# Kernel optimization log

Hardware: AMD Instinct MI355X
Metric: run time of the kernel (lower is better)

The kernel has to match this reference:

```python
import jax, jax.numpy as jnp
import numpy as np

N = 10000      # atoms
F = 32         # nr_atom_basis
H = 7          # nr_heads
C = F * H      # nr_coefficients = 224
E = 200000     # edges
NRBF = 50
CUTOFF = 5.0
EPS = 1e-8


def _seg_sum(x, idx, n):
    return jax.ops.segment_sum(x, idx, num_segments=n)


def _seg_mean(x, idx, n):
    # torch scatter_reduce 'mean' with include_self=False: sum/count, 0 for empty segments
    s = _seg_sum(x, idx, n)
    cnt = _seg_sum(jnp.ones((x.shape[0],), x.dtype), idx, n)
    cnt = jnp.maximum(cnt, 1.0).reshape((n,) + (1,) * (x.ndim - 1))
    return s / cnt


def _scatter_softmax(w, idx, n):
    m = jax.ops.segment_max(w, idx, num_segments=n)
    m = jnp.where(jnp.isfinite(m), m, 0.0)  # guard empty segments
    e = jnp.exp(w - m[idx])
    s = _seg_sum(e, idx, n)
    return e / s[idx]


def setup_inputs():
    key = jax.random.key(0)
    ks = jax.random.split(key, 16)
    def w(k, shape, scale=0.1):
        return jax.random.normal(k, shape, jnp.float32) * scale
    return {
        "h": w(ks[0], (N, F), 1.0),
        "x": w(ks[1], (N, 3), 1.0),
        "v": w(ks[2], (N, 3), 0.1),
        "pairlist": jax.random.randint(ks[3], (2, E), 0, N),
        "w_in": w(ks[4], (2 * F, NRBF)), "b_in": jnp.zeros((NRBF,), jnp.float32),
        "w_e1": w(ks[5], (2 * F + NRBF + 1, F)), "b_e1": jnp.zeros((F,), jnp.float32),
        "w_e2": w(ks[6], (F, F)), "b_e2": jnp.zeros((F,), jnp.float32),
        "w_att": w(ks[7], (F, H)), "b_att": jnp.zeros((H,), jnp.float32),
        "w_n1": w(ks[8], (F + C + F, F)), "b_n1": jnp.zeros((F,), jnp.float32),
        "w_n2": w(ks[9], (F, F)), "b_n2": jnp.zeros((F,), jnp.float32),
        "w_pn1": w(ks[10], (C, F)), "b_pn1": jnp.zeros((F,), jnp.float32),
        "w_pn2": w(ks[11], (F, F)), "b_pn2": jnp.zeros((F,), jnp.float32),
        "w_v1": w(ks[12], (F, F)), "b_v1": jnp.zeros((F,), jnp.float32),
        "w_v2": w(ks[13], (F, 1)),
        "w_xmix": w(ks[14], (C, C)),
        "w_vmix": w(ks[15], (C, 1)),
    }


def reference(h, x, v, pairlist, w_in, b_in, w_e1, b_e1, w_e2, b_e2,
              w_att, b_att, w_n1, b_n1, w_n2, b_n2, w_pn1, b_pn1,
              w_pn2, b_pn2, w_v1, b_v1, w_v2, w_xmix, w_vmix):
    act = jax.nn.silu
    idx_i, idx_j = pairlist[0], pairlist[1]
    n = h.shape[0]

    r_ij = x[idx_j] - x[idx_i]                      # [E,3]
    d_ij = jnp.linalg.norm(r_ij, axis=-1)           # [E]
    dir_ij = r_ij / (d_ij[:, None] + EPS)           # [E,3]

    # edge model: continuous-filter conv with concatenation
    h_cat = jnp.concatenate([h[idx_i], h[idx_j]], axis=-1)           # [E,2F]
    centers = jnp.linspace(0.0, CUTOFF, NRBF)
    width = centers[1] - centers[0]
    rbf = jnp.exp(-0.5 * ((d_ij[:, None] - centers) / width) ** 2)   # [E,NRBF]
    filt = rbf * (h_cat @ w_in + b_in)                               # [E,NRBF]
    edge_in = jnp.concatenate([h_cat, filt, d_ij[:, None]], axis=-1)
    h_ij_edge = act(edge_in @ w_e1 + b_e1) @ w_e2 + b_e2             # [E,F]

    # semantic attention (scatter softmax over edges grouped by idx_i)
    att_w = jax.nn.celu(h_ij_edge @ w_att + b_att, alpha=2.0)        # [E,H]
    cut = 0.5 * (jnp.cos(jnp.pi * d_ij / CUTOFF) + 1.0) * (d_ij < CUTOFF)
    att = _scatter_softmax(att_w * cut[:, None], idx_i, n)           # [E,H]
    # einsum('pf,ph->pfh').reshape -> f-major, h-minor
    h_ij_sem = (h_ij_edge[:, :, None] * att[:, None, :]).reshape(-1, C)  # [E,C]
    h_i_sem = _seg_sum(h_ij_sem, idx_i, n)                           # [N,C]

    # equivariant combinations + spatial attention
    comb = jnp.tanh(h_ij_sem @ w_xmix)[:, :, None] * dir_ij[:, None, :]  # [E,C,3]
    comb_mean = _seg_mean(comb, idx_i, n)                            # [N,C,3]
    cnsq = jnp.sum(comb_mean ** 2, axis=-1)                          # [N,C]
    h_i_spatial = act(act(cnsq @ w_pn1 + b_pn1) @ w_pn2 + b_pn2)     # [N,F]

    # node update
    node_in = jnp.concatenate([h, h_i_sem, h_i_spatial], axis=-1)
    h_upd = h + act(act(node_in @ w_n1 + b_n1) @ w_n2 + b_n2)        # [N,F]

    # velocity update
    v_ij = jnp.einsum('ecx,c->ex', comb, w_vmix[:, 0])               # [E,3]
    dv = _seg_mean(v_ij, idx_i, n)                                   # [N,3]
    gate = 2.0 * jax.nn.sigmoid(act(h @ w_v1 + b_v1) @ w_v2)         # [N,1]
    v_upd = gate * v + dv
    x_upd = x + v_upd
    return h_upd, x_upd, v_upd
```

## Files before the change

### kernel.cpp

```cpp
#include <hip/hip_runtime.h>
#include <hip/hip_bf16.h>
#include <math.h>

typedef unsigned short u16;
typedef __attribute__((ext_vector_type(8))) short bf16x8;
typedef __attribute__((ext_vector_type(4))) float f32x4;

constexpr int kF    = 32;
constexpr int kH    = 7;
constexpr int kC    = 224;
constexpr int kRBF  = 50;
constexpr int kM    = 128;
constexpr int kStr  = 232;
constexpr int kEM   = 128;
constexpr int kAStr = 136;
constexpr int kBStr = 40;
constexpr float kCut = 5.0f;
constexpr float kEps = 1e-8f;

__device__ __forceinline__ float silu_f(float a) { return a / (1.f + __expf(-a)); }
__device__ __forceinline__ float tanh_f(float x) {
    float e = __expf(2.f * x);
    return 1.f - 2.f / (e + 1.f);
}
__device__ __forceinline__ float bf2f(u16 u) {
    union { unsigned int i; float f; } v; v.i = ((unsigned int)u) << 16; return v.f;
}
__device__ __forceinline__ u16 f2bf(float f) {
    union { float f; unsigned int i; } v; v.f = f;
    unsigned int x = v.i;
    unsigned int round = ((x >> 16) & 1u) + 0x7fffu;
    return (u16)((x + round) >> 16);
}
__device__ __forceinline__ unsigned pk2(float a, float b) {
    union { __hip_bfloat162 h; unsigned u; } v;
    v.h = __float22bfloat162_rn(make_float2(a, b));
    return v.u;
}

__global__ __launch_bounds__(256) void init_kernel(
    const float* __restrict__ wx, const float* __restrict__ w_in,
    const float* __restrict__ w_e1, const float* __restrict__ w_e2,
    const float* __restrict__ w_att, const float* __restrict__ b_e2,
    const float* __restrict__ b_att,
    u16* __restrict__ wxT, u16* __restrict__ W1T, u16* __restrict__ W2T,
    u16* __restrict__ W3T, u16* __restrict__ W24T, float* __restrict__ b24,
    int* __restrict__ counts, int* __restrict__ cursor, int N_)
{
    int idx = blockIdx.x * 256 + threadIdx.x;
    if (idx < kC * kC) {
        int c = idx / kC, k = idx - c * kC;
        wxT[idx] = f2bf(wx[k * kC + c]);
    }
    if (idx < N_) { counts[idx] = 0; cursor[idx] = 0; }

    if (blockIdx.x == 0) {
        int t = threadIdx.x;
        for (int i = t; i < 64 * 64; i += 256) {
            int n = i >> 6, k = i & 63;
            W1T[i] = f2bf((n < kRBF) ? w_in[k * kRBF + n] : 0.f);
        }
        for (int i = t; i < 32 * 128; i += 256) {
            int n = i >> 7, k = i & 127;
            W2T[i] = f2bf((k < 115) ? w_e1[k * kF + n] : 0.f);
        }
        for (int i = t; i < 32 * 32; i += 256) {
            int n = i >> 5, k = i & 31;
            W3T[i] = f2bf(w_e2[k * kF + n]);
        }
        for (int i = t; i < 16 * 32; i += 256) {
            int n = i >> 5, k = i & 31;
            float a = 0.f;
            if (n < kH) for (int o = 0; o < kF; o++) a += w_e2[k * kF + o] * w_att[o * kH + n];
            W24T[i] = f2bf(a);
        }
        if (t < kH) {
            float a = b_att[t];
            for (int o = 0; o < kF; o++) a += b_e2[o] * w_att[o * kH + t];
            b24[t] = a;
        }
    }
}

__global__ __launch_bounds__(256) void hist_kernel(
    const int* __restrict__ pl, int* __restrict__ counts, int E_)
{
    int e = blockIdx.x * 256 + threadIdx.x;
    if (e < E_) atomicAdd(&counts[pl[e]], 1);
}

__global__ __launch_bounds__(1024) void scan_kernel(
    const int* __restrict__ counts, int* __restrict__ offsets, int n)
{
    __shared__ int buf[1024];
    int t = threadIdx.x;
    int chunk = (n + 1023) >> 10;
    int lo = t * chunk;
    int s = 0;
    for (int i = 0; i < chunk; i++) {
        int g = lo + i;
        if (g < n) s += counts[g];
    }
    buf[t] = s;
    __syncthreads();
    for (int off = 1; off < 1024; off <<= 1) {
        int v = (t >= off) ? buf[t - off] : 0;
        __syncthreads();
        buf[t] += v;
        __syncthreads();
    }
    int run = buf[t] - s;
    for (int i = 0; i < chunk; i++) {
        int g = lo + i;
        if (g < n) { offsets[g] = run; run += counts[g]; }
    }
    if (t == 1023) offsets[n] = buf[1023];
}

__global__ __launch_bounds__(256) void scatter_kernel(
    const int* __restrict__ pl, const int* __restrict__ offsets,
    int* __restrict__ cursor, int* __restrict__ rank, int* __restrict__ nid, int E_)
{
    int e = blockIdx.x * 256 + threadIdx.x;
    if (e < E_) {
        int i = pl[e];
        int p = atomicAdd(&cursor[i], 1);
        int pos = offsets[i] + p;
        rank[e] = pos;
        nid[pos] = i;
    }
}

__global__ __launch_bounds__(256) void edge_kernel(
    const float* __restrict__ h, const float* __restrict__ x,
    const int* __restrict__ pl, const int* __restrict__ rank_g, int E_,
    const float* __restrict__ b_in, const float* __restrict__ b_e1,
    const float* __restrict__ b_e2,
    const u16* __restrict__ W1T, const u16* __restrict__ W2T,
    const u16* __restrict__ W3T, const u16* __restrict__ W24T,
    const float* __restrict__ b24,
    float* __restrict__ he_g, float* __restrict__ logit_g,
    float* __restrict__ dir_g)
{
    __shared__ __align__(16) u16 s_A[kEM][kAStr];
    __shared__ __align__(16) u16 s_t1[kEM][kBStr];
    __shared__ float s_d[kEM];
    __shared__ int   s_r[kEM];

    int t = threadIdx.x;
    int T0 = blockIdx.x * kEM;
    int w = t >> 6, lane = t & 63, quad = lane >> 4, l15 = lane & 15;

    {
        int e = t >> 1, half = t & 1;
        int ge = T0 + e;
        bool val = ge < E_;
        int i = 0, j = 0;
        if (val) { i = pl[ge]; j = pl[E_ + ge]; }
        const float4* pi = (const float4*)(h + (size_t)i * kF) + half * 4;
        const float4* pj = (const float4*)(h + (size_t)j * kF) + half * 4;
#pragma unroll
        for (int q = 0; q < 4; q++) {
            float4 a = val ? pi[q] : make_float4(0.f, 0.f, 0.f, 0.f);
            float4 b = val ? pj[q] : make_float4(0.f, 0.f, 0.f, 0.f);
            unsigned* di = (unsigned*)&s_A[e][half * 16 + 4 * q];
            di[0] = pk2(a.x, a.y); di[1] = pk2(a.z, a.w);
            unsigned* dj = (unsigned*)&s_A[e][kF + half * 16 + 4 * q];
            dj[0] = pk2(b.x, b.y); dj[1] = pk2(b.z, b.w);
        }
        if (half == 0) {
            float d = 0.f;
            int r = 0;
            if (val) {
                r = rank_g[ge];
                float r0 = x[j * 3 + 0] - x[i * 3 + 0];
                float r1 = x[j * 3 + 1] - x[i * 3 + 1];
                float r2 = x[j * 3 + 2] - x[i * 3 + 2];
                d = sqrtf(r0 * r0 + r1 * r1 + r2 * r2);
                float inv = 1.0f / (d + kEps);
                dir_g[(size_t)r * 3 + 0] = r0 * inv;
                dir_g[(size_t)r * 3 + 1] = r1 * inv;
                dir_g[(size_t)r * 3 + 2] = r2 * inv;
            }
            s_r[e] = r;
            s_d[e] = d;
            s_A[e][114] = f2bf(d);
            s_A[e][115] = 0;
            unsigned* z = (unsigned*)&s_A[e][116];
#pragma unroll
            for (int q = 0; q < 6; q++) z[q] = 0u;
        }
    }
    __syncthreads();

    const float invw = 49.0f / kCut;

    {
        bf16x8 a1[2][2];
#pragma unroll
        for (int rt = 0; rt < 2; rt++)
#pragma unroll
            for (int kt = 0; kt < 2; kt++)
                a1[rt][kt] = *(const bf16x8*)&s_A[32 * w + 16 * rt + l15][kt * 32 + quad * 8];
#pragma unroll
        for (int ct = 0; ct < 4; ct++) {
            int c = ct * 16 + l15;
            bf16x8 b0 = *(const bf16x8*)(W1T + (size_t)c * 64 + quad * 8);
            bf16x8 b1 = *(const bf16x8*)(W1T + (size_t)c * 64 + 32 + quad * 8);
            float bin = (c < kRBF) ? b_in[c] : 0.f;
#pragma unroll
            for (int rt = 0; rt < 2; rt++) {
                f32x4 acc = {0.f, 0.f, 0.f, 0.f};
                acc = __builtin_amdgcn_mfma_f32_16x16x32_bf16(a1[rt][0], b0, acc, 0, 0, 0);
                acc = __builtin_amdgcn_mfma_f32_16x16x32_bf16(a1[rt][1], b1, acc, 0, 0, 0);
                if (c < kRBF) {
#pragma unroll
                    for (int r = 0; r < 4; r++) {
                        int row = 32 * w + 16 * rt + quad * 4 + r;
                        float arg = s_d[row] * invw - (float)c;
                        float filt = __expf(-0.5f * arg * arg) * (acc[r] + bin);
                        s_A[row][64 + c] = f2bf(filt);
                    }
                }
            }
        }
    }

    {
        bf16x8 a2[2][4];
#pragma unroll
        for (int rt = 0; rt < 2; rt++)
#pragma unroll
            for (int kt = 0; kt < 4; kt++)
                a2[rt][kt] = *(const bf16x8*)&s_A[32 * w + 16 * rt + l15][kt * 32 + quad * 8];
#pragma unroll
        for (int ct = 0; ct < 2; ct++) {
            int c = ct * 16 + l15;
            bf16x8 bb[4];
#pragma unroll
            for (int kt = 0; kt < 4; kt++)
                bb[kt] = *(const bf16x8*)(W2T + (size_t)c * 128 + kt * 32 + quad * 8);
            float be = b_e1[c];
#pragma unroll
            for (int rt = 0; rt < 2; rt++) {
                f32x4 acc = {0.f, 0.f, 0.f, 0.f};
#pragma unroll
                for (int kt = 0; kt < 4; kt++)
                    acc = __builtin_amdgcn_mfma_f32_16x16x32_bf16(a2[rt][kt], bb[kt], acc, 0, 0, 0);
#pragma unroll
                for (int r = 0; r < 4; r++) {
                    int row = 32 * w + 16 * rt + quad * 4 + r;
                    s_t1[row][c] = f2bf(silu_f(acc[r] + be));
                }
            }
        }
    }

    {
        bf16x8 a3[2];
#pragma unroll
        for (int rt = 0; rt < 2; rt++)
            a3[rt] = *(const bf16x8*)&s_t1[32 * w + 16 * rt + l15][quad * 8];

#pragma unroll
        for (int ct = 0; ct < 2; ct++) {
            int c = ct * 16 + l15;
            bf16x8 b3 = *(const bf16x8*)(W3T + (size_t)c * 32 + quad * 8);
            float be = b_e2[c];
#pragma unroll
            for (int rt = 0; rt < 2; rt++) {
                f32x4 acc = {0.f, 0.f, 0.f, 0.f};
                acc = __builtin_amdgcn_mfma_f32_16x16x32_bf16(a3[rt], b3, acc, 0, 0, 0);
#pragma unroll
                for (int r = 0; r < 4; r++) {
                    int row = 32 * w + 16 * rt + quad * 4 + r;
                    int ge = T0 + row;
                    if (ge < E_) he_g[(size_t)s_r[row] * kF + c] = acc[r] + be;
                }
            }
        }
        {
            bf16x8 b4 = *(const bf16x8*)(W24T + (size_t)l15 * 32 + quad * 8);
            float bb = (l15 < kH) ? b24[l15] : 0.f;
#pragma unroll
            for (int rt = 0; rt < 2; rt++) {
                f32x4 acc = {0.f, 0.f, 0.f, 0.f};
                acc = __builtin_amdgcn_mfma_f32_16x16x32_bf16(a3[rt], b4, acc, 0, 0, 0);
                if (l15 < kH) {
#pragma unroll
                    for (int r = 0; r < 4; r++) {
                        int row = 32 * w + 16 * rt + quad * 4 + r;
                        int ge = T0 + row;
                        if (ge < E_) {
                            float a = acc[r] + bb;
                            a = (a >= 0.f) ? a : 2.f * (__expf(0.5f * a) - 1.f);
                            float dd = s_d[row];
                            float cut = (dd < kCut)
                                ? 0.5f * (__cosf(0.62831853071795864f * dd) + 1.f) : 0.f;
                            logit_g[(size_t)s_r[row] * kH + l15] = a * cut;
                        }
                    }
                }
            }
        }
    }
}

__global__ __launch_bounds__(256) void stats_kernel(
    const float* __restrict__ logit_g, const int* __restrict__ offsets,
    float* __restrict__ m_g, float* __restrict__ invs_g, int N_)
{
    int wave = threadIdx.x >> 6;
    int lane = threadIdx.x & 63;
    int node = blockIdx.x * 4 + wave;
    if (node >= N_) return;
    int base = offsets[node];
    int deg  = offsets[node + 1] - base;

    float m[kH], ss[kH];
#pragma unroll
    for (int hh = 0; hh < kH; hh++) { m[hh] = -1e30f; ss[hh] = 0.f; }
    for (int e = lane; e < deg; e += 64) {
        const float* lp = logit_g + (size_t)(base + e) * kH;
#pragma unroll
        for (int hh = 0; hh < kH; hh++) {
            float vv = lp[hh];
            if (vv > m[hh]) { ss[hh] *= __expf(m[hh] - vv); m[hh] = vv; }
            ss[hh] += __expf(vv - m[hh]);
        }
    }
#pragma unroll
    for (int hh = 0; hh < kH; hh++) {
        float mm = m[hh], s2 = ss[hh];
#pragma unroll
        for (int off = 32; off >= 1; off >>= 1) {
            float mo = __shfl_xor(mm, off);
            float so = __shfl_xor(s2, off);
            float mn = fmaxf(mm, mo);
            s2 = s2 * __expf(mm - mn) + so * __expf(mo - mn);
            mm = mn;
        }
        if (lane == 0) {
            m_g[(size_t)node * kH + hh] = mm;
            invs_g[(size_t)node * kH + hh] = (s2 > 0.f) ? 1.f / s2 : 0.f;
        }
    }
}

__global__ __launch_bounds__(256) void xmix_kernel(
    const float* __restrict__ he_g, const float* __restrict__ logit_g,
    const float* __restrict__ dir_g, const int* __restrict__ nid,
    const float* __restrict__ m_g, const float* __restrict__ invs_g,
    const u16* __restrict__ wxT, int E_,
    float* __restrict__ nodeacc, float* __restrict__ bpart, int* __restrict__ bid)
{
    __shared__ __align__(16) u16 s_buf[kM][kStr];
    __shared__ float s_att[kM][kH];
    __shared__ __align__(16) float s_dir4[kM][4];
    __shared__ int   s_node[kM];
    __shared__ int   s_prev, s_next;

    int t = threadIdx.x;
    int T0 = blockIdx.x * kM;
    int cp = min(kM, E_ - T0);

    if (t < kM) s_node[t] = (T0 + t < E_) ? nid[T0 + t] : -1;
    if (t == 0) {
        s_prev = (T0 > 0) ? nid[T0 - 1] : -2;
        s_next = (T0 + cp < E_) ? nid[T0 + cp] : -2;
    }
    __syncthreads();

    int w    = t >> 6;
    int lane = t & 63;
    int quad = lane >> 4;
    int l15  = lane & 15;

    int ws = 32 * w;
    int we = min(ws + 32, cp);
    bool winvalid = (ws < cp);
    bool contL = false, contR = false;
    if (winvalid) {
        int nfirst = s_node[ws], nlast = s_node[we - 1];
        contL = (w == 0) ? (s_prev == nfirst) : (s_node[ws - 1] == nfirst);
        contR = (we == cp) ? (s_next == nlast) : (s_node[we] == nlast);
    }
    if (lane == 0) {
        int b0 = -1, b1 = -1;
        if (winvalid) {
            int nfirst = s_node[ws], nlast = s_node[we - 1];
            b0 = contL ? nfirst : -1;
            if (contR && !(nfirst == nlast && contL)) b1 = nlast;
        }
        bid[8 * blockIdx.x + 2 * w + 0] = b0;
        bid[8 * blockIdx.x + 2 * w + 1] = b1;
    }
    bool active_w = winvalid && (lane < 56);
    int c0 = 4 * lane;

    for (int idx = t; idx < kM * kH; idx += 256) {
        int e = idx / kH, hh = idx - e * kH;
        float a = 0.f;
        if (T0 + e < E_) {
            int nd = s_node[e];
            a = __expf(logit_g[(size_t)(T0 + e) * kH + hh] - m_g[(size_t)nd * kH + hh])
                * invs_g[(size_t)nd * kH + hh];
        }
        s_att[e][hh] = a;
    }
    for (int idx = t; idx < cp * 3; idx += 256) {
        int e = idx / 3, xx = idx - e * 3;
        s_dir4[e][xx] = dir_g[(size_t)(T0 + e) * 3 + xx];
    }
    __syncthreads();

#pragma unroll
    for (int p = 0; p < kM * kF / 256; p++) {
        int idx = t + 256 * p;
        int e = idx >> 5, f = idx & 31;
        float hv = (T0 + e < E_) ? he_g[(size_t)(T0 + e) * kF + f] : 0.f;
        float sv[7];
#pragma unroll
        for (int hh = 0; hh < kH; hh++) sv[hh] = hv * s_att[e][hh];
        u16* dst = &s_buf[e][f * 7];
        if ((f & 1) == 0) {
            *(unsigned*)(dst)     = pk2(sv[0], sv[1]);
            *(unsigned*)(dst + 2) = pk2(sv[2], sv[3]);
            *(unsigned*)(dst + 4) = pk2(sv[4], sv[5]);
            dst[6] = f2bf(sv[6]);
        } else {
            dst[0] = f2bf(sv[0]);
            *(unsigned*)(dst + 1) = pk2(sv[1], sv[2]);
            *(unsigned*)(dst + 3) = pk2(sv[3], sv[4]);
            *(unsigned*)(dst + 5) = pk2(sv[5], sv[6]);
        }
    }
    __syncthreads();

    if (active_w) {
        float hs0 = 0.f, hs1 = 0.f, hs2 = 0.f, hs3 = 0.f;
        int rs = ws;
        for (int e = ws; e < we; e++) {
            if (s_node[e] != s_node[rs]) {
                bool comp = (rs > ws) || !contL;
                float4 vv = make_float4(hs0, hs1, hs2, hs3);
                if (comp) *(float4*)&nodeacc[(size_t)s_node[rs] * 896 + 672 + c0] = vv;
                else *(float4*)&bpart[(size_t)(8 * blockIdx.x + 2 * w) * 896 + 672 + c0] = vv;
                hs0 = hs1 = hs2 = hs3 = 0.f; rs = e;
            }
            uint2 pv = *(const uint2*)&s_buf[e][c0];
            hs0 += bf2f((u16)pv.x); hs1 += bf2f((u16)(pv.x >> 16));
            hs2 += bf2f((u16)pv.y); hs3 += bf2f((u16)(pv.y >> 16));
        }
        bool t0 = (rs == ws);
        bool comp = ((!t0) || !contL) && !contR;
        float4 vv = make_float4(hs0, hs1, hs2, hs3);
        if (comp) *(float4*)&nodeacc[(size_t)s_node[rs] * 896 + 672 + c0] = vv;
        else {
            int slot = (t0 && contL) ? 0 : 1;
            *(float4*)&bpart[(size_t)(8 * blockIdx.x + 2 * w + slot) * 896 + 672 + c0] = vv;
        }
    }

    bf16x8 afr[2][7];
#pragma unroll
    for (int rt = 0; rt < 2; rt++)
#pragma unroll
        for (int kt = 0; kt < 7; kt++)
            afr[rt][kt] = *(const bf16x8*)&s_buf[32 * w + 16 * rt + l15][kt * 32 + quad * 8];

    bf16x8 bA[7], bB[7];
    {
        const u16* bp = wxT + (size_t)l15 * kC + quad * 8;
#pragma unroll
        for (int kt = 0; kt < 7; kt++) bA[kt] = *(const bf16x8*)(bp + kt * 32);
    }
    __syncthreads();

    for (int ct = 0; ct < 14; ct++) {
        bf16x8* cur = (ct & 1) ? bB : bA;
        bf16x8* nxt = (ct & 1) ? bA : bB;
        if (ct < 13) {
            const u16* bp = wxT + (size_t)((ct + 1) * 16 + l15) * kC + quad * 8;
#pragma unroll
            for (int kt = 0; kt < 7; kt++) nxt[kt] = *(const bf16x8*)(bp + kt * 32);
        }
        f32x4 acc0 = {0.f, 0.f, 0.f, 0.f};
        f32x4 acc1 = {0.f, 0.f, 0.f, 0.f};
#pragma unroll
        for (int kt = 0; kt < 7; kt++) {
            acc0 = __builtin_amdgcn_mfma_f32_16x16x32_bf16(afr[0][kt], cur[kt], acc0, 0, 0, 0);
            acc1 = __builtin_amdgcn_mfma_f32_16x16x32_bf16(afr[1][kt], cur[kt], acc1, 0, 0, 0);
        }
        int colg = ct * 16 + l15;
#pragma unroll
        for (int s = 0; s < 2; s++) {
            f32x4 ac = s ? acc1 : acc0;
            int rbase = 32 * w + 16 * s + quad * 4;
            unsigned p01 = pk2(tanh_f(ac[0]), tanh_f(ac[1]));
            unsigned p23 = pk2(tanh_f(ac[2]), tanh_f(ac[3]));
            s_buf[rbase + 0][colg] = (u16)p01;
            s_buf[rbase + 1][colg] = (u16)(p01 >> 16);
            s_buf[rbase + 2][colg] = (u16)p23;
            s_buf[rbase + 3][colg] = (u16)(p23 >> 16);
        }
    }
    __syncthreads();

    if (active_w) {
        float a0[4] = {0.f, 0.f, 0.f, 0.f};
        float a1[4] = {0.f, 0.f, 0.f, 0.f};
        float a2[4] = {0.f, 0.f, 0.f, 0.f};
        int rs = ws;
        for (int e = ws; e < we; e++) {
            if (s_node[e] != s_node[rs]) {
                bool comp = (rs > ws) || !contL;
                float* p = comp ? (nodeacc + (size_t)s_node[rs] * 896)
                                : (bpart + (size_t)(8 * blockIdx.x + 2 * w) * 896);
                *(float4*)&p[c0]       = make_float4(a0[0], a0[1], a0[2], a0[3]);
                *(float4*)&p[224 + c0] = make_float4(a1[0], a1[1], a1[2], a1[3]);
                *(float4*)&p[448 + c0] = make_float4(a2[0], a2[1], a2[2], a2[3]);
#pragma unroll
                for (int q = 0; q < 4; q++) { a0[q] = 0.f; a1[q] = 0.f; a2[q] = 0.f; }
                rs = e;
            }
            float4 dd = *(const float4*)&s_dir4[e][0];
            uint2 pv = *(const uint2*)&s_buf[e][c0];
            float Tv[4];
            Tv[0] = bf2f((u16)pv.x); Tv[1] = bf2f((u16)(pv.x >> 16));
            Tv[2] = bf2f((u16)pv.y); Tv[3] = bf2f((u16)(pv.y >> 16));
#pragma unroll
            for (int q = 0; q < 4; q++) {
                a0[q] += Tv[q] * dd.x;
                a1[q] += Tv[q] * dd.y;
                a2[q] += Tv[q] * dd.z;
            }
        }
        bool t0 = (rs == ws);
        bool comp = ((!t0) || !contL) && !contR;
        float* p;
        if (comp) p = nodeacc + (size_t)s_node[rs] * 896;
        else {
            int slot = (t0 && contL) ? 0 : 1;
            p = bpart + (size_t)(8 * blockIdx.x + 2 * w + slot) * 896;
        }
        *(float4*)&p[c0]       = make_float4(a0[0], a0[1], a0[2], a0[3]);
        *(float4*)&p[224 + c0] = make_float4(a1[0], a1[1], a1[2], a1[3]);
        *(float4*)&p[448 + c0] = make_float4(a2[0], a2[1], a2[2], a2[3]);
    }
}

__global__ __launch_bounds__(256) void node_kernel(
    const float* __restrict__ h, const float* __restrict__ x, const float* __restrict__ v,
    const float* __restrict__ nodeacc, const float* __restrict__ bpart,
    const int* __restrict__ bid, const int* __restrict__ offs,
    const float* __restrict__ w_n1, const float* __restrict__ b_n1,
    const float* __restrict__ w_n2, const float* __restrict__ b_n2,
    const float* __restrict__ w_pn1, const float* __restrict__ b_pn1,
    const float* __restrict__ w_pn2, const float* __restrict__ b_pn2,
    const float* __restrict__ w_v1, const float* __restrict__ b_v1,
    const float* __restrict__ w_v2, const float* __restrict__ w_vmix,
    float* __restrict__ out_h, float* __restrict__ out_x, float* __restrict__ out_v,
    int N_)
{
    __shared__ float s_cm[4][3][kC];
    __shared__ float s_cnsq[4][kC];
    __shared__ float s_ni[4][288];
    __shared__ float s_part[8][4][kF];
    __shared__ float s_hn[4][kF], s_sp1[4][kF], s_spat[4][kF], s_n1v[4][kF], s_g1[4][kF];
    __shared__ float s_pdv[4][3][8];
    __shared__ float s_gate[4], s_dv[4][3];

    int t = threadIdx.x;
    int n0 = blockIdx.x * 4;

    if (t < kC) {
        for (int nd = 0; nd < 4; nd++) {
            int node = n0 + nd;
            if (node >= N_) break;
            int base = offs[node], end = offs[node + 1];
            int deg = end - base;
            float a0 = 0.f, a1 = 0.f, a2 = 0.f, hh = 0.f;
            if (deg > 0) {
                int wlo = base >> 5, whi = (end - 1) >> 5;
                if (wlo == whi) {
                    const float* p = nodeacc + (size_t)node * 896;
                    a0 = p[t]; a1 = p[224 + t]; a2 = p[448 + t]; hh = p[672 + t];
                } else {
                    for (int W = wlo; W <= whi; W++) {
#pragma unroll
                        for (int s = 0; s < 2; s++) {
                            if (bid[2 * W + s] == node) {
                                const float* p = bpart + (size_t)(2 * W + s) * 896;
                                a0 += p[t]; a1 += p[224 + t]; a2 += p[448 + t]; hh += p[672 + t];
                            }
                        }
                    }
                }
            }
            float invc = 1.f / fmaxf((float)deg, 1.f);
            float m0 = a0 * invc, m1 = a1 * invc, m2 = a2 * invc;
            s_cm[nd][0][t] = m0; s_cm[nd][1][t] = m1; s_cm[nd][2][t] = m2;
            s_cnsq[nd][t] = m0 * m0 + m1 * m1 + m2 * m2;
            s_ni[nd][kF + t] = hh;
        }
    } else {
        int ln = t - 224;
        for (int nd = 0; nd < 4; nd++) {
            int node = n0 + nd;
            float hv = (node < N_) ? h[(size_t)node * kF + ln] : 0.f;
            s_hn[nd][ln] = hv;
            s_ni[nd][ln] = hv;
        }
    }
    __syncthreads();

    int o = t & 31, g = t >> 5;
    {
        float acc[4] = {0.f, 0.f, 0.f, 0.f};
        int cb = g * 28;
        for (int i = 0; i < 28; i++) {
            float wv = w_pn1[(cb + i) * kF + o];
#pragma unroll
            for (int nd = 0; nd < 4; nd++) acc[nd] += s_cnsq[nd][cb + i] * wv;
        }
#pragma unroll
        for (int nd = 0; nd < 4; nd++) s_part[g][nd][o] = acc[nd];
    }
    __syncthreads();
    if (t < 128) {
        int nd = t >> 5;
        float a = b_pn1[o];
#pragma unroll
        for (int g2 = 0; g2 < 8; g2++) a += s_part[g2][nd][o];
        s_sp1[nd][o] = silu_f(a);
    } else {
        int nd = (t - 128) >> 5;
        float a = b_v1[o];
        for (int f = 0; f < kF; f++) a += s_hn[nd][f] * w_v1[f * kF + o];
        s_g1[nd][o] = silu_f(a);
    }
    __syncthreads();
    if (t < 128) {
        int nd = t >> 5;
        float a = b_pn2[o];
        for (int o2 = 0; o2 < kF; o2++) a += s_sp1[nd][o2] * w_pn2[o2 * kF + o];
        s_spat[nd][o] = silu_f(a);
    } else if (t < 132) {
        int nd = t - 128;
        float a = 0.f;
        for (int o2 = 0; o2 < kF; o2++) a += s_g1[nd][o2] * w_v2[o2];
        s_gate[nd] = 2.f / (1.f + __expf(-a));
    } else if (t >= 160) {
        int q = t - 160; int nd = q / 24; int r = q - nd * 24;
        int xx = r >> 3, ln = r & 7;
        float a = 0.f;
        for (int c = ln; c < kC; c += 8) a += w_vmix[c] * s_cm[nd][xx][c];
        s_pdv[nd][xx][ln] = a;
    }
    __syncthreads();
    if (t < 128) {
        int nd = t >> 5;
        s_ni[nd][kF + kC + o] = s_spat[nd][o];
    } else if (t < 140) {
        int q = t - 128; int nd = q / 3; int xx = q - nd * 3;
        float a = 0.f;
#pragma unroll
        for (int ln = 0; ln < 8; ln++) a += s_pdv[nd][xx][ln];
        s_dv[nd][xx] = a;
    }
    __syncthreads();
    {
        float acc[4] = {0.f, 0.f, 0.f, 0.f};
        int rb = g * 36;
        for (int i = 0; i < 36; i++) {
            float wv = w_n1[(rb + i) * kF + o];
#pragma unroll
            for (int nd = 0; nd < 4; nd++) acc[nd] += s_ni[nd][rb + i] * wv;
        }
#pragma unroll
        for (int nd = 0; nd < 4; nd++) s_part[g][nd][o] = acc[nd];
    }
    __syncthreads();
    if (t < 128) {
        int nd = t >> 5;
        float a = b_n1[o];
#pragma unroll
        for (int g2 = 0; g2 < 8; g2++) a += s_part[g2][nd][o];
        s_n1v[nd][o] = silu_f(a);
    }
    __syncthreads();
    if (t < 128) {
        int nd = t >> 5; int node = n0 + nd;
        if (node < N_) {
            float a = b_n2[o];
            for (int o2 = 0; o2 < kF; o2++) a += s_n1v[nd][o2] * w_n2[o2 * kF + o];
            out_h[(size_t)node * kF + o] = s_hn[nd][o] + silu_f(a);
        }
    } else if (t < 140) {
        int q = t - 128; int nd = q / 3; int xx = q - nd * 3;
        int node = n0 + nd;
        if (node < N_) {
            float vv = v[(size_t)node * 3 + xx];
            float vu = s_gate[nd] * vv + s_dv[nd][xx];
            out_v[(size_t)node * 3 + xx] = vu;
            out_x[(size_t)node * 3 + xx] = x[(size_t)node * 3 + xx] + vu;
        }
    }
}

extern "C" void kernel_launch(void* const* d_in, const int* in_sizes, int n_in,
                              void* d_out, int out_size, void* d_ws, size_t ws_size,
                              hipStream_t stream)
{
    const float* h      = (const float*)d_in[0];
    const float* x      = (const float*)d_in[1];
    const float* v      = (const float*)d_in[2];
    const int*   pl     = (const int*)d_in[3];
    const float* w_in   = (const float*)d_in[4];
    const float* b_in   = (const float*)d_in[5];
    const float* w_e1   = (const float*)d_in[6];
    const float* b_e1   = (const float*)d_in[7];
    const float* w_e2   = (const float*)d_in[8];
    const float* b_e2   = (const float*)d_in[9];
    const float* w_att  = (const float*)d_in[10];
    const float* b_att  = (const float*)d_in[11];
    const float* w_n1   = (const float*)d_in[12];
    const float* b_n1   = (const float*)d_in[13];
    const float* w_n2   = (const float*)d_in[14];
    const float* b_n2   = (const float*)d_in[15];
    const float* w_pn1  = (const float*)d_in[16];
    const float* b_pn1  = (const float*)d_in[17];
    const float* w_pn2  = (const float*)d_in[18];
    const float* b_pn2  = (const float*)d_in[19];
    const float* w_v1   = (const float*)d_in[20];
    const float* b_v1   = (const float*)d_in[21];
    const float* w_v2   = (const float*)d_in[22];
    const float* w_xmix = (const float*)d_in[23];
    const float* w_vmix = (const float*)d_in[24];

    const int E_ = in_sizes[3] / 2;
    const int N_ = in_sizes[0] / kF;
    const int nblk = (E_ + kM - 1) / kM;

    char* w = (char*)d_ws;
    u16*   wxT     = (u16*)w;   w += (size_t)kC * kC * 2;
    u16*   W1T     = (u16*)w;   w += (size_t)64 * 64 * 2;
    u16*   W2T     = (u16*)w;   w += (size_t)32 * 128 * 2;
    u16*   W3T     = (u16*)w;   w += (size_t)32 * 32 * 2;
    u16*   W24T    = (u16*)w;   w += (size_t)16 * 32 * 2;
    float* b24     = (float*)w; w += 8 * 4;
    float* he_g    = (float*)w; w += (size_t)E_ * kF * 4;
    float* logit_g = (float*)w; w += (size_t)E_ * kH * 4;
    float* dir_g   = (float*)w; w += (size_t)E_ * 3 * 4;
    float* m_g     = (float*)w; w += (size_t)N_ * kH * 4;
    float* invs_g  = (float*)w; w += (size_t)N_ * kH * 4;
    float* nodeacc = (float*)w; w += (size_t)N_ * 896 * 4;
    float* bpart   = (float*)w; w += (size_t)8 * nblk * 896 * 4;
    int*   bid     = (int*)w;   w += (size_t)8 * nblk * 4;
    int* counts    = (int*)w;   w += (size_t)N_ * 4;
    int* offs      = (int*)w;   w += (size_t)(N_ + 1) * 4;
    int* cursor    = (int*)w;   w += (size_t)N_ * 4;
    int* rank_g    = (int*)w;   w += (size_t)E_ * 4;
    int* nid       = (int*)w;   w += (size_t)E_ * 4;

    float* out_h = (float*)d_out;
    float* out_x = out_h + (size_t)N_ * kF;
    float* out_v = out_x + (size_t)N_ * 3;

    init_kernel<<<dim3((kC * kC + 255) / 256), dim3(256), 0, stream>>>(
        w_xmix, w_in, w_e1, w_e2, w_att, b_e2, b_att,
        wxT, W1T, W2T, W3T, W24T, b24, counts, cursor, N_);

    hist_kernel<<<dim3((E_ + 255) / 256), dim3(256), 0, stream>>>(pl, counts, E_);

    scan_kernel<<<dim3(1), dim3(1024), 0, stream>>>(counts, offs, N_);

    scatter_kernel<<<dim3((E_ + 255) / 256), dim3(256), 0, stream>>>(
        pl, offs, cursor, rank_g, nid, E_);

    edge_kernel<<<dim3((E_ + kEM - 1) / kEM), dim3(256), 0, stream>>>(
        h, x, pl, rank_g, E_, b_in, b_e1, b_e2, W1T, W2T, W3T, W24T, b24,
        he_g, logit_g, dir_g);

    stats_kernel<<<dim3((N_ + 3) / 4), dim3(256), 0, stream>>>(
        logit_g, offs, m_g, invs_g, N_);

    xmix_kernel<<<dim3(nblk), dim3(256), 0, stream>>>(
        he_g, logit_g, dir_g, nid, m_g, invs_g, wxT, E_,
        nodeacc, bpart, bid);

    node_kernel<<<dim3((N_ + 3) / 4), dim3(256), 0, stream>>>(
        h, x, v, nodeacc, bpart, bid, offs,
        w_n1, b_n1, w_n2, b_n2, w_pn1, b_pn1, w_pn2, b_pn2,
        w_v1, b_v1, w_v2, w_vmix, out_h, out_x, out_v, N_);
}
```

Baseline: 361.6 us.

## Fuse histogram into init kernel and split xmix MFMA rows over eight waves

The edge-count histogram now runs inside init_kernel as a grid-stride loop, and the counters are zeroed with memsets, which removes one kernel launch. xmix_kernel now launches 512 threads per block, so each of 8 waves computes a 16-row MFMA tile instead of 4 waves computing 32 rows each. This lowers per-wave register use and the serial MFMA chain, giving more latency hiding. The segment-reduction phase still uses only the first 4 waves, so half the block sits idle there. Relying on the memset happening before init_kernel's atomics depends on stream ordering.

```diff
diff --git a/kernel.cpp b/kernel.cpp
--- a/kernel.cpp
+++ b/kernel.cpp
@@ -42,17 +42,17 @@
     const float* __restrict__ wx, const float* __restrict__ w_in,
     const float* __restrict__ w_e1, const float* __restrict__ w_e2,
     const float* __restrict__ w_att, const float* __restrict__ b_e2,
-    const float* __restrict__ b_att,
+    const float* __restrict__ b_att, const int* __restrict__ pl,
     u16* __restrict__ wxT, u16* __restrict__ W1T, u16* __restrict__ W2T,
     u16* __restrict__ W3T, u16* __restrict__ W24T, float* __restrict__ b24,
-    int* __restrict__ counts, int* __restrict__ cursor, int N_)
+    int* __restrict__ counts, int E_)
 {
     int idx = blockIdx.x * 256 + threadIdx.x;
     if (idx < kC * kC) {
         int c = idx / kC, k = idx - c * kC;
         wxT[idx] = f2bf(wx[k * kC + c]);
     }
-    if (idx < N_) { counts[idx] = 0; cursor[idx] = 0; }
+    for (int e = idx; e < E_; e += gridDim.x * 256) atomicAdd(&counts[pl[e]], 1);
 
     if (blockIdx.x == 0) {
         int t = threadIdx.x;
@@ -80,13 +80,6 @@
             b24[t] = a;
         }
     }
-}
-
-__global__ __launch_bounds__(256) void hist_kernel(
-    const int* __restrict__ pl, int* __restrict__ counts, int E_)
-{
-    int e = blockIdx.x * 256 + threadIdx.x;
-    if (e < E_) atomicAdd(&counts[pl[e]], 1);
 }
 
 __global__ __launch_bounds__(1024) void scan_kernel(
@@ -347,7 +340,7 @@
     }
 }
 
-__global__ __launch_bounds__(256) void xmix_kernel(
+__global__ __launch_bounds__(512, 4) void xmix_kernel(
     const float* __restrict__ he_g, const float* __restrict__ logit_g,
     const float* __restrict__ dir_g, const int* __restrict__ nid,
     const float* __restrict__ m_g, const float* __restrict__ invs_g,
@@ -378,14 +371,14 @@
 
     int ws = 32 * w;
     int we = min(ws + 32, cp);
-    bool winvalid = (ws < cp);
+    bool winvalid = (w < 4) && (ws < cp);
     bool contL = false, contR = false;
     if (winvalid) {
         int nfirst = s_node[ws], nlast = s_node[we - 1];
         contL = (w == 0) ? (s_prev == nfirst) : (s_node[ws - 1] == nfirst);
         contR = (we == cp) ? (s_next == nlast) : (s_node[we] == nlast);
     }
-    if (lane == 0) {
+    if (w < 4 && lane == 0) {
         int b0 = -1, b1 = -1;
         if (winvalid) {
             int nfirst = s_node[ws], nlast = s_node[we - 1];
@@ -398,7 +391,7 @@
     bool active_w = winvalid && (lane < 56);
     int c0 = 4 * lane;
 
-    for (int idx = t; idx < kM * kH; idx += 256) {
+    for (int idx = t; idx < kM * kH; idx += 512) {
         int e = idx / kH, hh = idx - e * kH;
         float a = 0.f;
         if (T0 + e < E_) {
@@ -408,15 +401,15 @@
         }
         s_att[e][hh] = a;
     }
-    for (int idx = t; idx < cp * 3; idx += 256) {
+    for (int idx = t; idx < cp * 3; idx += 512) {
         int e = idx / 3, xx = idx - e * 3;
         s_dir4[e][xx] = dir_g[(size_t)(T0 + e) * 3 + xx];
     }
     __syncthreads();
 
 #pragma unroll
-    for (int p = 0; p < kM * kF / 256; p++) {
-        int idx = t + 256 * p;
+    for (int p = 0; p < kM * kF / 512; p++) {
+        int idx = t + 512 * p;
         int e = idx >> 5, f = idx & 31;
         float hv = (T0 + e < E_) ? he_g[(size_t)(T0 + e) * kF + f] : 0.f;
         float sv[7];
@@ -462,12 +455,10 @@
         }
     }
 
-    bf16x8 afr[2][7];
-#pragma unroll
-    for (int rt = 0; rt < 2; rt++)
-#pragma unroll
-        for (int kt = 0; kt < 7; kt++)
-            afr[rt][kt] = *(const bf16x8*)&s_buf[32 * w + 16 * rt + l15][kt * 32 + quad * 8];
+    bf16x8 afr[7];
+#pragma unroll
+    for (int kt = 0; kt < 7; kt++)
+        afr[kt] = *(const bf16x8*)&s_buf[16 * w + l15][kt * 32 + quad * 8];
 
     bf16x8 bA[7], bB[7];
     {
@@ -485,25 +476,18 @@
 #pragma unroll
             for (int kt = 0; kt < 7; kt++) nxt[kt] = *(const bf16x8*)(bp + kt * 32);
         }
-        f32x4 acc0 = {0.f, 0.f, 0.f, 0.f};
-        f32x4 acc1 = {0.f, 0.f, 0.f, 0.f};
-#pragma unroll
-        for (int kt = 0; kt < 7; kt++) {
-            acc0 = __builtin_amdgcn_mfma_f32_16x16x32_bf16(afr[0][kt], cur[kt], acc0, 0, 0, 0);
-            acc1 = __builtin_amdgcn_mfma_f32_16x16x32_bf16(afr[1][kt], cur[kt], acc1, 0, 0, 0);
-        }
+        f32x4 acc = {0.f, 0.f, 0.f, 0.f};
+#pragma unroll
+        for (int kt = 0; kt < 7; kt++)
+            acc = __builtin_amdgcn_mfma_f32_16x16x32_bf16(afr[kt], cur[kt], acc, 0, 0, 0);
         int colg = ct * 16 + l15;
-#pragma unroll
-        for (int s = 0; s < 2; s++) {
-            f32x4 ac = s ? acc1 : acc0;
-            int rbase = 32 * w + 16 * s + quad * 4;
-            unsigned p01 = pk2(tanh_f(ac[0]), tanh_f(ac[1]));
-            unsigned p23 = pk2(tanh_f(ac[2]), tanh_f(ac[3]));
-            s_buf[rbase + 0][colg] = (u16)p01;
-            s_buf[rbase + 1][colg] = (u16)(p01 >> 16);
-            s_buf[rbase + 2][colg] = (u16)p23;
-            s_buf[rbase + 3][colg] = (u16)(p23 >> 16);
-        }
+        int rbase = 16 * w + quad * 4;
+        unsigned p01 = pk2(tanh_f(acc[0]), tanh_f(acc[1]));
+        unsigned p23 = pk2(tanh_f(acc[2]), tanh_f(acc[3]));
+        s_buf[rbase + 0][colg] = (u16)p01;
+        s_buf[rbase + 1][colg] = (u16)(p01 >> 16);
+        s_buf[rbase + 2][colg] = (u16)p23;
+        s_buf[rbase + 3][colg] = (u16)(p23 >> 16);
     }
     __syncthreads();
 
@@ -768,11 +752,12 @@
     float* out_x = out_h + (size_t)N_ * kF;
     float* out_v = out_x + (size_t)N_ * 3;
 
+    hipMemsetAsync(counts, 0, (size_t)N_ * 4, stream);
+    hipMemsetAsync(cursor, 0, (size_t)N_ * 4, stream);
+
     init_kernel<<<dim3((kC * kC + 255) / 256), dim3(256), 0, stream>>>(
-        w_xmix, w_in, w_e1, w_e2, w_att, b_e2, b_att,
-        wxT, W1T, W2T, W3T, W24T, b24, counts, cursor, N_);
-
-    hist_kernel<<<dim3((E_ + 255) / 256), dim3(256), 0, stream>>>(pl, counts, E_);
+        w_xmix, w_in, w_e1, w_e2, w_att, b_e2, b_att, pl,
+        wxT, W1T, W2T, W3T, W24T, b24, counts, E_);
 
     scan_kernel<<<dim3(1), dim3(1024), 0, stream>>>(counts, offs, N_);
 
@@ -786,7 +771,7 @@
     stats_kernel<<<dim3((N_ + 3) / 4), dim3(256), 0, stream>>>(
         logit_g, offs, m_g, invs_g, N_);
 
-    xmix_kernel<<<dim3(nblk), dim3(256), 0, stream>>>(
+    xmix_kernel<<<dim3(nblk), dim3(512), 0, stream>>>(
         he_g, logit_g, dir_g, nid, m_g, invs_g, wxT, E_,
         nodeacc, bpart, bid);
 
```

After: 370.8 us. +2.5%, slower.

## Fuse histogram into init kernel and triple-buffer wxT prefetch in xmix

Applied to the files above, without the earlier changes.

Zeroing of counts and cursor moves to hipMemsetAsync calls, and the edge histogram atomics are folded into init_kernel with a grid-stride loop, removing the separate hist_kernel launch. In xmix_kernel the B-operand prefetch of the transposed w_xmix tiles goes from double to triple buffering with a fully unrolled column loop, so loads are issued two tiles ahead. This adds two memset operations and raises register pressure from the third 7-fragment buffer, which could reduce occupancy.

```diff
diff --git a/kernel.cpp b/kernel.cpp
--- a/kernel.cpp
+++ b/kernel.cpp
@@ -42,17 +42,17 @@
     const float* __restrict__ wx, const float* __restrict__ w_in,
     const float* __restrict__ w_e1, const float* __restrict__ w_e2,
     const float* __restrict__ w_att, const float* __restrict__ b_e2,
-    const float* __restrict__ b_att,
+    const float* __restrict__ b_att, const int* __restrict__ pl,
     u16* __restrict__ wxT, u16* __restrict__ W1T, u16* __restrict__ W2T,
     u16* __restrict__ W3T, u16* __restrict__ W24T, float* __restrict__ b24,
-    int* __restrict__ counts, int* __restrict__ cursor, int N_)
+    int* __restrict__ counts, int E_)
 {
     int idx = blockIdx.x * 256 + threadIdx.x;
     if (idx < kC * kC) {
         int c = idx / kC, k = idx - c * kC;
         wxT[idx] = f2bf(wx[k * kC + c]);
     }
-    if (idx < N_) { counts[idx] = 0; cursor[idx] = 0; }
+    for (int e = idx; e < E_; e += gridDim.x * 256) atomicAdd(&counts[pl[e]], 1);
 
     if (blockIdx.x == 0) {
         int t = threadIdx.x;
@@ -80,13 +80,6 @@
             b24[t] = a;
         }
     }
-}
-
-__global__ __launch_bounds__(256) void hist_kernel(
-    const int* __restrict__ pl, int* __restrict__ counts, int E_)
-{
-    int e = blockIdx.x * 256 + threadIdx.x;
-    if (e < E_) atomicAdd(&counts[pl[e]], 1);
 }
 
 __global__ __launch_bounds__(1024) void scan_kernel(
@@ -469,28 +462,30 @@
         for (int kt = 0; kt < 7; kt++)
             afr[rt][kt] = *(const bf16x8*)&s_buf[32 * w + 16 * rt + l15][kt * 32 + quad * 8];
 
-    bf16x8 bA[7], bB[7];
-    {
-        const u16* bp = wxT + (size_t)l15 * kC + quad * 8;
-#pragma unroll
-        for (int kt = 0; kt < 7; kt++) bA[kt] = *(const bf16x8*)(bp + kt * 32);
-    }
-    __syncthreads();
-
+    bf16x8 bb[3][7];
+#pragma unroll
+    for (int kt = 0; kt < 7; kt++)
+        bb[0][kt] = *(const bf16x8*)(wxT + (size_t)l15 * kC + kt * 32 + quad * 8);
+#pragma unroll
+    for (int kt = 0; kt < 7; kt++)
+        bb[1][kt] = *(const bf16x8*)(wxT + (size_t)(16 + l15) * kC + kt * 32 + quad * 8);
+    __syncthreads();
+
+#pragma unroll
     for (int ct = 0; ct < 14; ct++) {
-        bf16x8* cur = (ct & 1) ? bB : bA;
-        bf16x8* nxt = (ct & 1) ? bA : bB;
-        if (ct < 13) {
-            const u16* bp = wxT + (size_t)((ct + 1) * 16 + l15) * kC + quad * 8;
-#pragma unroll
-            for (int kt = 0; kt < 7; kt++) nxt[kt] = *(const bf16x8*)(bp + kt * 32);
+        const int cur = ct % 3;
+        const int nxt = (ct + 2) % 3;
+        if (ct < 12) {
+            const u16* bp = wxT + (size_t)((ct + 2) * 16 + l15) * kC + quad * 8;
+#pragma unroll
+            for (int kt = 0; kt < 7; kt++) bb[nxt][kt] = *(const bf16x8*)(bp + kt * 32);
         }
         f32x4 acc0 = {0.f, 0.f, 0.f, 0.f};
         f32x4 acc1 = {0.f, 0.f, 0.f, 0.f};
 #pragma unroll
         for (int kt = 0; kt < 7; kt++) {
-            acc0 = __builtin_amdgcn_mfma_f32_16x16x32_bf16(afr[0][kt], cur[kt], acc0, 0, 0, 0);
-            acc1 = __builtin_amdgcn_mfma_f32_16x16x32_bf16(afr[1][kt], cur[kt], acc1, 0, 0, 0);
+            acc0 = __builtin_amdgcn_mfma_f32_16x16x32_bf16(afr[0][kt], bb[cur][kt], acc0, 0, 0, 0);
+            acc1 = __builtin_amdgcn_mfma_f32_16x16x32_bf16(afr[1][kt], bb[cur][kt], acc1, 0, 0, 0);
         }
         int colg = ct * 16 + l15;
 #pragma unroll
@@ -768,11 +763,12 @@
     float* out_x = out_h + (size_t)N_ * kF;
     float* out_v = out_x + (size_t)N_ * 3;
 
+    hipMemsetAsync(counts, 0, (size_t)N_ * 4, stream);
+    hipMemsetAsync(cursor, 0, (size_t)N_ * 4, stream);
+
     init_kernel<<<dim3((kC * kC + 255) / 256), dim3(256), 0, stream>>>(
-        w_xmix, w_in, w_e1, w_e2, w_att, b_e2, b_att,
-        wxT, W1T, W2T, W3T, W24T, b24, counts, cursor, N_);
-
-    hist_kernel<<<dim3((E_ + 255) / 256), dim3(256), 0, stream>>>(pl, counts, E_);
+        w_xmix, w_in, w_e1, w_e2, w_att, b_e2, b_att, pl,
+        wxT, W1T, W2T, W3T, W24T, b24, counts, E_);
 
     scan_kernel<<<dim3(1), dim3(1024), 0, stream>>>(counts, offs, N_);
 
```

Result: faster. 348.4 us (-3.7%).
